# Kernel optimization log

Hardware: AMD Instinct MI355X
Metric: run time of the kernel (lower is better)

## Reference

```python
import jax, jax.numpy as jnp
import numpy as np
from jax import lax

B, T0, H0, W0 = 8, 8, 14, 14
C, NH = 768, 8
D = C // NH            # head_dim = 96
N = T0 * H0 * W0 + 1   # 1569 tokens incl. cls
SCALE = D ** -0.5
EPS = 1e-5


def _pool_norm(xh, conv_w, ln_g, ln_b, thw, stride):
    """AttentionPool with depthwise conv3d + LayerNorm. xh: [B, NH, N, D]."""
    cls_tok, xs = xh[:, :, :1, :], xh[:, :, 1:, :]
    b, n, _, d = xs.shape
    t, h, w = thw
    # (b n) c t h w
    xs = xs.reshape(b * n, t, h, w, d).transpose(0, 4, 1, 2, 3)
    y = lax.conv_general_dilated(
        xs, conv_w, window_strides=stride,
        padding=[(1, 1), (1, 1), (1, 1)],
        feature_group_count=d,
        dimension_numbers=("NCDHW", "OIDHW", "NCDHW"))
    ot, oh, ow = y.shape[2], y.shape[3], y.shape[4]
    y = y.transpose(0, 2, 3, 4, 1).reshape(b, n, ot * oh * ow, d)
    y = jnp.concatenate([cls_tok, y], axis=2)
    mu = y.mean(-1, keepdims=True)
    var = y.var(-1, keepdims=True)
    y = (y - mu) * lax.rsqrt(var + EPS) * ln_g + ln_b
    return y, (ot, oh, ow)


def setup_inputs() -> dict:
    key = jax.random.key(0)
    ks = jax.random.split(key, 12)
    s = lambda fan: (1.0 / np.sqrt(fan))
    return {
        "x": jax.random.normal(ks[0], (B, N, C), jnp.float32),
        "W_qkv": jax.random.normal(ks[1], (C, 3 * C), jnp.float32) * s(C),
        "b_qkv": jnp.zeros((3 * C,), jnp.float32),
        "W_proj": jax.random.normal(ks[2], (C, C), jnp.float32) * s(C),
        "b_proj": jnp.zeros((C,), jnp.float32),
        "conv_q_w": jax.random.normal(ks[3], (D, 1, 3, 3, 3), jnp.float32) * s(27),
        "conv_k_w": jax.random.normal(ks[4], (D, 1, 3, 3, 3), jnp.float32) * s(27),
        "conv_v_w": jax.random.normal(ks[5], (D, 1, 3, 3, 3), jnp.float32) * s(27),
        "lnq_g": jnp.ones((D,), jnp.float32), "lnq_b": jnp.zeros((D,), jnp.float32),
        "lnk_g": jnp.ones((D,), jnp.float32), "lnk_b": jnp.zeros((D,), jnp.float32),
        "lnv_g": jnp.ones((D,), jnp.float32), "lnv_b": jnp.zeros((D,), jnp.float32),
        "t": T0, "h": H0, "w": W0,
    }


def reference(x, W_qkv, b_qkv, W_proj, b_proj,
              conv_q_w, conv_k_w, conv_v_w,
              lnq_g, lnq_b, lnk_g, lnk_b, lnv_g, lnv_b,
              t, h, w):
    thw = (int(t), int(h), int(w))
    Bx, Nx, Cx = x.shape
    qkv = x @ W_qkv + b_qkv                       # [B, N, 3C]
    qkv = qkv.reshape(Bx, Nx, 3, NH, D).transpose(2, 0, 3, 1, 4)  # qkv b h n d
    q, k, v = qkv[0], qkv[1], qkv[2]
    q, q_shape = _pool_norm(q, conv_q_w, lnq_g, lnq_b, thw, (1, 1, 1))
    k, _ = _pool_norm(k, conv_k_w, lnk_g, lnk_b, thw, (1, 2, 2))
    v, _ = _pool_norm(v, conv_v_w, lnv_g, lnv_b, thw, (1, 2, 2))
    dots = jnp.einsum("bhid,bhjd->bhij", q, k) * SCALE
    attn = jax.nn.softmax(dots, axis=-1)
    out = jnp.einsum("bhij,bhjd->bhid", attn, v)  # [B, NH, Nq, D]
    out = out.transpose(0, 2, 1, 3).reshape(Bx, -1, Cx)
    out = out @ W_proj + b_proj
    return out
```

## Files before the change

### kernel.cpp

```cpp
#include <hip/hip_runtime.h>
#include <hip/hip_bf16.h>
#include <math.h>

#define B_   8
#define NH_  8
#define D_   96
#define C_   768
#define N_   1569
#define NKV_ 393
#define M_   (B_*N_)
#define QKV1 ((size_t)B_*NH_*N_*D_)
#define QPAD 1664
#define KPAD 416
#define SCALE_ 0.10206207261596575f

using short8v = __attribute__((ext_vector_type(8))) short;
using f32x4   = __attribute__((ext_vector_type(4))) float;
using f32x2   = __attribute__((ext_vector_type(2))) float;
typedef unsigned short u16;

#define GLOAD_LDS16(g, l) __builtin_amdgcn_global_load_lds( \
    (const __attribute__((address_space(1))) void*)(g),     \
    (__attribute__((address_space(3))) void*)(l), 16, 0, 0)

static __device__ __forceinline__ u16 f2bf(float f) {
    __hip_bfloat16 b = __float2bfloat16(f);
    return *(u16*)&b;
}

static __device__ __forceinline__ unsigned xcd_swizzle(unsigned orig, unsigned nwg) {
    const unsigned qq = nwg >> 3, rr = nwg & 7;
    const unsigned xcd = orig & 7, loc = orig >> 3;
    return (xcd < rr ? xcd * (qq + 1) : rr * (qq + 1) + (xcd - rr) * qq) + loc;
}

__global__ __launch_bounds__(256)
void cvt_f32_to_bf16(const float* __restrict__ in, u16* __restrict__ out, int n4)
{
    const int i = blockIdx.x * 256 + threadIdx.x;
    if (i < n4) {
        const float4 v = ((const float4*)in)[i];
        ushort4 o;
        o.x = f2bf(v.x); o.y = f2bf(v.y); o.z = f2bf(v.z); o.w = f2bf(v.w);
        ((ushort4*)out)[i] = o;
    }
}

__global__ __launch_bounds__(256)
void transpose_cvt(const float* __restrict__ W, u16* __restrict__ Wt, int ncols)
{
    __shared__ float tile[32][33];
    const int tx = threadIdx.x & 31, ty = threadIdx.x >> 5;
    const int n0 = blockIdx.x * 32, k0 = blockIdx.y * 32;
    #pragma unroll
    for (int i = 0; i < 4; ++i)
        tile[ty + i * 8][tx] = W[(size_t)(k0 + ty + i * 8) * ncols + n0 + tx];
    __syncthreads();
    #pragma unroll
    for (int i = 0; i < 4; ++i)
        Wt[(size_t)(n0 + ty + i * 8) * 768 + k0 + tx] = f2bf(tile[tx][ty + i * 8]);
}

__global__ __launch_bounds__(256)
void transpose_w(const float* __restrict__ cwq, const float* __restrict__ cwk,
                 const float* __restrict__ cwv, float* __restrict__ outT)
{
    const int i = blockIdx.x * 256 + threadIdx.x;
    if (i < 3 * 27 * 96) {
        const int tsr = i / 2592;
        const int r = i - tsr * 2592;
        const int tap = r / 96, ch = r - tap * 96;
        const float* src = tsr == 0 ? cwq : (tsr == 1 ? cwk : cwv);
        outT[i] = src[ch * 27 + tap];
    }
}

__global__ __launch_bounds__(256)
void zero_pad_vt(u16* __restrict__ vt)
{
    const int i = blockIdx.x * 256 + threadIdx.x;
    const int total = 64 * 96 * (KPAD - NKV_);
    if (i < total) {
        const int j = i % (KPAD - NKV_);
        const int rest = i / (KPAD - NKV_);
        vt[(size_t)rest * KPAD + NKV_ + j] = 0;
    }
}

template<int NC, bool SCATTER>
__global__ __launch_bounds__(512)
void gemm_bf16_kernel(const u16* __restrict__ A, const u16* __restrict__ Bt,
                      const float* __restrict__ bias, void* __restrict__ outp)
{
    constexpr int NXT = NC / 128;
    __shared__ alignas(16) u16 As[2][128 * 64];
    __shared__ alignas(16) u16 Bs[2][128 * 64];

    const int tid  = threadIdx.x;
    const int w    = tid >> 6, lane = tid & 63;
    const int c    = lane & 15, g = lane >> 4;
    const int wm   = w >> 2, wn = w & 3;
    const int lrow = lane >> 3, lcol = lane & 7;

    const unsigned wg = xcd_swizzle(blockIdx.x, gridDim.x);
    const int m0 = (int)(wg / NXT) * 128;
    const int n0 = (int)(wg % NXT) * 128;

    f32x4 acc[4][2];
    #pragma unroll
    for (int i = 0; i < 4; ++i)
        #pragma unroll
        for (int j = 0; j < 2; ++j) acc[i][j] = (f32x4){0.f, 0.f, 0.f, 0.f};

#define STAGE(BUF, K0) do {                                                      \
    _Pragma("unroll")                                                            \
    for (int t = 0; t < 2; ++t) {                                                \
        const int r = t * 64 + w * 8;                                            \
        const int row = r + lrow;                                                \
        const int scol = (lcol ^ (row & 7)) * 8;                                 \
        int m = m0 + row; if (m >= M_) m = M_ - 1;                               \
        GLOAD_LDS16(&A[(size_t)m * 768 + (K0) + scol], &As[BUF][r * 64]);        \
        GLOAD_LDS16(&Bt[(size_t)(n0 + row) * 768 + (K0) + scol],                 \
                    &Bs[BUF][r * 64]);                                           \
    } } while (0)

    const int xora = (g ^ (c & 7)) * 8;
    const int xorb = ((4 + g) ^ (c & 7)) * 8;

#define KSTEP(BUF, LAST, PREF, KNEXT) do {                                       \
    if (LAST) asm volatile("s_waitcnt vmcnt(0)" ::: "memory");                   \
    else      asm volatile("s_waitcnt vmcnt(4)" ::: "memory");                   \
    __builtin_amdgcn_s_barrier();                                                \
    short8v a0[4], a1[4], b0[2], b1[2];                                          \
    _Pragma("unroll")                                                            \
    for (int i = 0; i < 4; ++i) {                                                \
        const int ra = (wm * 64 + i * 16 + c) * 64;                              \
        a0[i] = *(const short8v*)&As[BUF][ra + xora];                            \
        a1[i] = *(const short8v*)&As[BUF][ra + xorb];                            \
    }                                                                            \
    _Pragma("unroll")                                                            \
    for (int j = 0; j < 2; ++j) {                                                \
        const int rb = (wn * 32 + j * 16 + c) * 64;                              \
        b0[j] = *(const short8v*)&Bs[BUF][rb + xora];                            \
        b1[j] = *(const short8v*)&Bs[BUF][rb + xorb];                            \
    }                                                                            \
    asm volatile("s_waitcnt lgkmcnt(0)" ::: "memory");                           \
    __builtin_amdgcn_sched_barrier(0);                                           \
    __builtin_amdgcn_s_barrier();                                                \
    if (PREF) STAGE(BUF, KNEXT);                                                 \
    __builtin_amdgcn_s_setprio(1);                                               \
    _Pragma("unroll")                                                            \
    for (int i = 0; i < 4; ++i)                                                  \
        _Pragma("unroll")                                                        \
        for (int j = 0; j < 2; ++j)                                              \
            acc[i][j] = __builtin_amdgcn_mfma_f32_16x16x32_bf16(                 \
                a0[i], b0[j], acc[i][j], 0, 0, 0);                               \
    _Pragma("unroll")                                                            \
    for (int i = 0; i < 4; ++i)                                                  \
        _Pragma("unroll")                                                        \
        for (int j = 0; j < 2; ++j)                                              \
            acc[i][j] = __builtin_amdgcn_mfma_f32_16x16x32_bf16(                 \
                a1[i], b1[j], acc[i][j], 0, 0, 0);                               \
    __builtin_amdgcn_s_setprio(0);                                               \
    } while (0)

    STAGE(0, 0);
    STAGE(1, 64);
    #pragma unroll
    for (int tt = 0; tt < 5; ++tt) {
        KSTEP(0, false, true, (2 * tt + 2) * 64);
        KSTEP(1, false, true, (2 * tt + 3) * 64);
    }
    KSTEP(0, false, false, 0);
    KSTEP(1, true,  false, 0);
#undef STAGE
#undef KSTEP

    #pragma unroll
    for (int i = 0; i < 4; ++i) {
        const int mrow = m0 + wm * 64 + i * 16 + g * 4;
        #pragma unroll
        for (int j = 0; j < 2; ++j) {
            const int ncol = n0 + wn * 32 + j * 16 + c;
            const float bv = bias[ncol];
            if constexpr (SCATTER) {
                u16* out = (u16*)outp;
                const int s   = ncol / C_;
                const int rem = ncol - s * C_;
                const int hh  = rem / D_;
                const int dd  = rem - hh * D_;
                #pragma unroll
                for (int r = 0; r < 4; ++r) {
                    const int m = mrow + r;
                    if (m < M_) {
                        const int bb2 = m / N_;
                        const int n = m - bb2 * N_;
                        out[(size_t)s * QKV1 +
                            ((size_t)(bb2 * NH_ + hh) * N_ + n) * D_ + dd] = f2bf(acc[i][j][r] + bv);
                    }
                }
            } else {
                float* out = (float*)outp;
                #pragma unroll
                for (int r = 0; r < 4; ++r) {
                    const int m = mrow + r;
                    if (m < M_) out[(size_t)m * NC + ncol] = acc[i][j][r] + bv;
                }
            }
        }
    }
}

static __device__ __forceinline__ void loadx6(const u16* __restrict__ rowp,
                                              int iw, f32x2 x[3])
{
    if (iw < 0 || iw >= 14) {
        x[0] = x[1] = x[2] = (f32x2){0.f, 0.f};
        return;
    }
    const unsigned* p = (const unsigned*)(rowp + (size_t)iw * 96);
    #pragma unroll
    for (int j = 0; j < 3; ++j) {
        const unsigned u = p[j];
        x[j][0] = __uint_as_float(u << 16);
        x[j][1] = __uint_as_float(u & 0xffff0000u);
    }
}

template<int STRIDE, int OHW, int WMODE, int WO0>
static __device__ __forceinline__
void pool_task(const u16* __restrict__ in, const float* __restrict__ cwT,
               const float* __restrict__ g, const float* __restrict__ bta,
               u16* __restrict__ out, int tokstride, int bh, int to, int ho,
               float oscale)
{
    const int sl = threadIdx.x & 15;
    const u16* base = in + (size_t)bh * N_ * 96 + 6 * sl;

    f32x2 acc[7][3];
    #pragma unroll
    for (int i = 0; i < 7; ++i)
        #pragma unroll
        for (int p = 0; p < 3; ++p) acc[i][p] = (f32x2){0.f, 0.f};

    #pragma unroll
    for (int dt = 0; dt < 3; ++dt) {
        const int t = to - 1 + dt;
        if (t < 0 || t > 7) continue;
        #pragma unroll
        for (int dh = 0; dh < 3; ++dh) {
            const int h = ho * STRIDE - 1 + dh;
            if (h < 0 || h >= 14) continue;
            const int tapb = dt * 9 + dh * 3;
            f32x2 wt[3][3];
            #pragma unroll
            for (int dw = 0; dw < 3; ++dw)
                #pragma unroll
                for (int p = 0; p < 3; ++p)
                    wt[dw][p] = *(const f32x2*)&cwT[(tapb + dw) * 96 + 6 * sl + 2 * p];
            const u16* rowp = base + (size_t)(1 + t * 196 + h * 14) * 96;

            if constexpr (STRIDE == 1) {
                f32x2 xm[3], x0[3], xp[3];
                loadx6(rowp, WO0 - 1, xm);
                loadx6(rowp, WO0, x0);
                #pragma unroll
                for (int wo = 0; wo < 7; ++wo) {
                    loadx6(rowp, WO0 + wo + 1, xp);
                    #pragma unroll
                    for (int p = 0; p < 3; ++p) {
                        acc[wo][p] = __builtin_elementwise_fma(wt[0][p], xm[p], acc[wo][p]);
                        acc[wo][p] = __builtin_elementwise_fma(wt[1][p], x0[p], acc[wo][p]);
                        acc[wo][p] = __builtin_elementwise_fma(wt[2][p], xp[p], acc[wo][p]);
                        xm[p] = x0[p]; x0[p] = xp[p];
                    }
                }
            } else {
                #pragma unroll
                for (int wo = 0; wo < 7; ++wo) {
                    #pragma unroll
                    for (int dw = 0; dw < 3; ++dw) {
                        f32x2 xa[3];
                        loadx6(rowp, 2 * wo - 1 + dw, xa);
                        #pragma unroll
                        for (int p = 0; p < 3; ++p)
                            acc[wo][p] = __builtin_elementwise_fma(wt[dw][p], xa[p], acc[wo][p]);
                    }
                }
            }
        }
    }

    f32x2 gg[3], bb[3];
    #pragma unroll
    for (int p = 0; p < 3; ++p) {
        gg[p] = *(const f32x2*)&g[6 * sl + 2 * p] * oscale;
        bb[p] = *(const f32x2*)&bta[6 * sl + 2 * p] * oscale;
    }

    #pragma unroll
    for (int wo = 0; wo < 7; ++wo) {
        float s = acc[wo][0][0] + acc[wo][0][1] + acc[wo][1][0] + acc[wo][1][1]
                + acc[wo][2][0] + acc[wo][2][1];
        float sq = acc[wo][0][0] * acc[wo][0][0];
        sq = fmaf(acc[wo][0][1], acc[wo][0][1], sq);
        sq = fmaf(acc[wo][1][0], acc[wo][1][0], sq);
        sq = fmaf(acc[wo][1][1], acc[wo][1][1], sq);
        sq = fmaf(acc[wo][2][0], acc[wo][2][0], sq);
        sq = fmaf(acc[wo][2][1], acc[wo][2][1], sq);
        #pragma unroll
        for (int off = 1; off < 16; off <<= 1) {
            s  += __shfl_xor(s, off, 64);
            sq += __shfl_xor(sq, off, 64);
        }
        const float mu = s * (1.f / 96.f);
        const float rstd = rsqrtf(sq * (1.f / 96.f) - mu * mu + 1e-5f);
        const f32x2 muv = (f32x2){mu, mu};
        const int tok = 1 + (to * OHW + ho) * OHW + WO0 + wo;
        u16 yb[6];
        #pragma unroll
        for (int p = 0; p < 3; ++p) {
            const f32x2 y = (acc[wo][p] - muv) * rstd * gg[p] + bb[p];
            yb[2 * p] = f2bf(y[0]); yb[2 * p + 1] = f2bf(y[1]);
        }
        if constexpr (WMODE == 2) {
            #pragma unroll
            for (int j = 0; j < 6; ++j)
                out[((size_t)bh * 96 + 6 * sl + j) * KPAD + tok] = yb[j];
        } else {
            unsigned* op = (unsigned*)&out[((size_t)bh * tokstride + tok) * 96 + 6 * sl];
            #pragma unroll
            for (int p = 0; p < 3; ++p)
                op[p] = (unsigned)yb[2 * p] | ((unsigned)yb[2 * p + 1] << 16);
        }
    }
}

template<int WMODE>
static __device__ __forceinline__
void pool_cls_v5(const u16* __restrict__ in, const float* __restrict__ g,
                 const float* __restrict__ bta, u16* __restrict__ out,
                 int tokstride, int bh, float oscale)
{
    const int sl = threadIdx.x & 15;
    const unsigned* p = (const unsigned*)(in + (size_t)bh * N_ * 96 + 6 * sl);
    f32x2 v[3];
    #pragma unroll
    for (int j = 0; j < 3; ++j) {
        const unsigned u = p[j];
        v[j][0] = __uint_as_float(u << 16);
        v[j][1] = __uint_as_float(u & 0xffff0000u);
    }
    float s = v[0][0] + v[0][1] + v[1][0] + v[1][1] + v[2][0] + v[2][1];
    float sq = v[0][0]*v[0][0] + v[0][1]*v[0][1] + v[1][0]*v[1][0]
             + v[1][1]*v[1][1] + v[2][0]*v[2][0] + v[2][1]*v[2][1];
    #pragma unroll
    for (int off = 1; off < 16; off <<= 1) {
        s  += __shfl_xor(s, off, 64);
        sq += __shfl_xor(sq, off, 64);
    }
    const float mu = s * (1.f / 96.f);
    const float rstd = rsqrtf(sq * (1.f / 96.f) - mu * mu + 1e-5f);
    u16 yb[6];
    #pragma unroll
    for (int p2 = 0; p2 < 3; ++p2) {
        const f32x2 gg = *(const f32x2*)&g[6 * sl + 2 * p2] * oscale;
        const f32x2 bb = *(const f32x2*)&bta[6 * sl + 2 * p2] * oscale;
        const f32x2 y = (v[p2] - (f32x2){mu, mu}) * rstd * gg + bb;
        yb[2 * p2] = f2bf(y[0]); yb[2 * p2 + 1] = f2bf(y[1]);
    }
    if constexpr (WMODE == 2) {
        #pragma unroll
        for (int j = 0; j < 6; ++j)
            out[((size_t)bh * 96 + 6 * sl + j) * KPAD] = yb[j];
    } else {
        unsigned* op = (unsigned*)&out[(size_t)bh * tokstride * 96 + 6 * sl];
        #pragma unroll
        for (int p2 = 0; p2 < 3; ++p2)
            op[p2] = (unsigned)yb[2 * p2] | ((unsigned)yb[2 * p2 + 1] << 16);
    }
}

#define NTASKS 21696
__global__ __launch_bounds__(256)
void pool_ln_v5_kernel(const u16* __restrict__ qin, const u16* __restrict__ kin,
                       const u16* __restrict__ vin, const float* __restrict__ cwT,
                       const float* __restrict__ gq, const float* __restrict__ bq,
                       const float* __restrict__ gk, const float* __restrict__ bk,
                       const float* __restrict__ gv, const float* __restrict__ bv,
                       u16* __restrict__ qout, u16* __restrict__ kout,
                       u16* __restrict__ vtout)
{
    const unsigned wg = xcd_swizzle(blockIdx.x, gridDim.x);
    const int gid = (int)(wg * 16 + (threadIdx.x >> 4));
    if (gid >= NTASKS) return;

    if (gid < 14336) {
        const int chunk = gid / 7168;
        const int r = gid - chunk * 7168;
        const int ho = r % 14;
        const int to = (r / 14) & 7;
        const int bh = r / 112;
        if (chunk == 0)
            pool_task<1, 14, 0, 0>(qin, cwT, gq, bq, qout, QPAD, bh, to, ho, SCALE_);
        else
            pool_task<1, 14, 0, 7>(qin, cwT, gq, bq, qout, QPAD, bh, to, ho, SCALE_);
    } else if (gid < 17920) {
        const int r = gid - 14336;
        const int ho = r % 7;
        const int to = (r / 7) & 7;
        const int bh = r / 56;
        pool_task<2, 7, 0, 0>(kin, cwT + 2592, gk, bk, kout, KPAD, bh, to, ho, 1.f);
    } else if (gid < 21504) {
        const int r = gid - 17920;
        const int ho = r % 7;
        const int to = (r / 7) & 7;
        const int bh = r / 56;
        pool_task<2, 7, 2, 0>(vin, cwT + 5184, gv, bv, vtout, KPAD, bh, to, ho, 1.f);
    } else {
        const int r = gid - 21504;
        const int tsr = r >> 6, bh = r & 63;
        if (tsr == 0)      pool_cls_v5<0>(qin, gq, bq, qout, QPAD, bh, SCALE_);
        else if (tsr == 1) pool_cls_v5<0>(kin, gk, bk, kout, KPAD, bh, 1.f);
        else               pool_cls_v5<2>(vin, gv, bv, vtout, KPAD, bh, 1.f);
    }
}

__global__ __launch_bounds__(256)
void attn_mfma_kernel(const u16* __restrict__ Q, const u16* __restrict__ K,
                      const u16* __restrict__ VT, u16* __restrict__ Out)
{
    __shared__ alignas(16) u16 plds[4][2][512];
    const int tid  = threadIdx.x;
    const int w    = tid >> 6, lane = tid & 63;
    const int c    = lane & 15, g = lane >> 4;

    const unsigned wg = xcd_swizzle(blockIdx.x, gridDim.x);
    const int bh = (int)(wg / 13);
    const int b  = bh >> 3, hh = bh & 7;
    const int q0 = (int)(wg % 13) * 128 + w * 32;

    const size_t qbase = (size_t)bh * QPAD * 96;
    const size_t kbase = (size_t)bh * KPAD * 96;

    short8v qa[2][3];
    #pragma unroll
    for (int s2 = 0; s2 < 2; ++s2)
        #pragma unroll
        for (int kf = 0; kf < 3; ++kf)
            qa[s2][kf] = *(const short8v*)
                &Q[qbase + (size_t)(q0 + s2 * 16 + c) * 96 + kf * 32 + g * 8];

    f32x4 oacc[2][6];
    #pragma unroll
    for (int s2 = 0; s2 < 2; ++s2)
        #pragma unroll
        for (int t = 0; t < 6; ++t) oacc[s2][t] = (f32x4){0.f, 0.f, 0.f, 0.f};
    float lsum[2][4] = {{0.f,0.f,0.f,0.f},{0.f,0.f,0.f,0.f}};

    short8v kb[2][6];
#define LOADK(IDX, PR) do {                                                     \
    _Pragma("unroll")                                                           \
    for (int h = 0; h < 2; ++h)                                                 \
        _Pragma("unroll")                                                       \
        for (int kf = 0; kf < 3; ++kf)                                          \
            kb[IDX][h * 3 + kf] = *(const short8v*)                             \
                &K[kbase + (size_t)((PR) * 32 + h * 16 + c) * 96 + kf * 32 + g * 8]; \
    } while (0)

    LOADK(0, 0);

    #pragma unroll
    for (int pr = 0; pr < 13; ++pr) {
        const int cur = pr & 1, nxt = cur ^ 1;

        short8v vt[6];
        #pragma unroll
        for (int t = 0; t < 6; ++t)
            vt[t] = *(const short8v*)
                &VT[kbase + (size_t)(t * 16 + c) * KPAD + pr * 32 + g * 8];

        f32x4 sacc[2][2];
        __builtin_amdgcn_s_setprio(1);
        #pragma unroll
        for (int s2 = 0; s2 < 2; ++s2)
            #pragma unroll
            for (int h = 0; h < 2; ++h) {
                f32x4 sa = (f32x4){0.f, 0.f, 0.f, 0.f};
                sa = __builtin_amdgcn_mfma_f32_16x16x32_bf16(qa[s2][0], kb[cur][h*3+0], sa, 0, 0, 0);
                sa = __builtin_amdgcn_mfma_f32_16x16x32_bf16(qa[s2][1], kb[cur][h*3+1], sa, 0, 0, 0);
                sa = __builtin_amdgcn_mfma_f32_16x16x32_bf16(qa[s2][2], kb[cur][h*3+2], sa, 0, 0, 0);
                sacc[s2][h] = sa;
            }
        __builtin_amdgcn_s_setprio(0);

        if (pr < 12) LOADK(nxt, pr + 1);

        #pragma unroll
        for (int s2 = 0; s2 < 2; ++s2)
            #pragma unroll
            for (int h = 0; h < 2; ++h) {
                const int jcol = pr * 32 + h * 16 + c;
                #pragma unroll
                for (int r = 0; r < 4; ++r) {
                    float s = sacc[s2][h][r];
                    if (jcol >= NKV_) s = -1e30f;
                    const float p = __expf(s);
                    lsum[s2][r] += p;
                    const int q    = g * 4 + r;
                    const int j    = h * 16 + c;
                    const int dstL = q | ((j >> 3) << 4);
                    plds[w][s2][dstL * 8 + (j & 7)] = f2bf(p);
                }
            }
        asm volatile("s_waitcnt lgkmcnt(0)" ::: "memory");
        __builtin_amdgcn_sched_barrier(0);
        const short8v pa0 = *(const short8v*)&plds[w][0][lane * 8];
        const short8v pa1 = *(const short8v*)&plds[w][1][lane * 8];

        __builtin_amdgcn_s_setprio(1);
        #pragma unroll
        for (int t = 0; t < 6; ++t)
            oacc[0][t] = __builtin_amdgcn_mfma_f32_16x16x32_bf16(pa0, vt[t], oacc[0][t], 0, 0, 0);
        #pragma unroll
        for (int t = 0; t < 6; ++t)
            oacc[1][t] = __builtin_amdgcn_mfma_f32_16x16x32_bf16(pa1, vt[t], oacc[1][t], 0, 0, 0);
        __builtin_amdgcn_s_setprio(0);
    }
#undef LOADK

    float linv[2][4];
    #pragma unroll
    for (int s2 = 0; s2 < 2; ++s2)
        #pragma unroll
        for (int r = 0; r < 4; ++r) {
            float s = lsum[s2][r];
            s += __shfl_xor(s, 1, 64);
            s += __shfl_xor(s, 2, 64);
            s += __shfl_xor(s, 4, 64);
            s += __shfl_xor(s, 8, 64);
            linv[s2][r] = 1.f / s;
        }

    #pragma unroll
    for (int s2 = 0; s2 < 2; ++s2)
        #pragma unroll
        for (int t = 0; t < 6; ++t)
            #pragma unroll
            for (int r = 0; r < 4; ++r) {
                const int row = q0 + s2 * 16 + g * 4 + r;
                if (row < N_)
                    Out[((size_t)(b * N_ + row)) * 768 + hh * 96 + t * 16 + c] =
                        f2bf(oacc[s2][t][r] * linv[s2][r]);
            }
}

extern "C" void kernel_launch(void* const* d_in, const int* in_sizes, int n_in,
                              void* d_out, int out_size, void* d_ws, size_t ws_size,
                              hipStream_t stream)
{
    const float* x     = (const float*)d_in[0];
    const float* Wqkv  = (const float*)d_in[1];
    const float* bqkv  = (const float*)d_in[2];
    const float* Wproj = (const float*)d_in[3];
    const float* bproj = (const float*)d_in[4];
    const float* cwq   = (const float*)d_in[5];
    const float* cwk   = (const float*)d_in[6];
    const float* cwv   = (const float*)d_in[7];
    const float* lnqg  = (const float*)d_in[8];
    const float* lnqb  = (const float*)d_in[9];
    const float* lnkg  = (const float*)d_in[10];
    const float* lnkb  = (const float*)d_in[11];
    const float* lnvg  = (const float*)d_in[12];
    const float* lnvb  = (const float*)d_in[13];

    u16* ws = (u16*)d_ws;
    u16* qkv_raw = ws;
    u16* q16 = qkv_raw + 3 * QKV1;
    u16* k16 = q16 + (size_t)64 * QPAD * 96;
    u16* vt16 = k16 + (size_t)64 * KPAD * 96;
    u16* x16    = vt16 + (size_t)64 * KPAD * 96;
    u16* Wqkvt  = x16 + (size_t)M_ * 768;
    u16* Wprojt = Wqkvt + (size_t)2304 * 768;
    float* cwT  = (float*)(Wprojt + (size_t)768 * 768);
    u16* attn16 = qkv_raw;
    float* out = (float*)d_out;

    cvt_f32_to_bf16<<<(M_ * 768 / 4 + 255) / 256, 256, 0, stream>>>(x, x16, M_ * 768 / 4);
    transpose_cvt<<<dim3(2304 / 32, 768 / 32), 256, 0, stream>>>(Wqkv, Wqkvt, 2304);
    transpose_cvt<<<dim3(768 / 32, 768 / 32), 256, 0, stream>>>(Wproj, Wprojt, 768);
    transpose_w<<<(3 * 27 * 96 + 255) / 256, 256, 0, stream>>>(cwq, cwk, cwv, cwT);
    zero_pad_vt<<<(64 * 96 * (KPAD - NKV_) + 255) / 256, 256, 0, stream>>>(vt16);

    gemm_bf16_kernel<2304, true><<<18 * 99, 512, 0, stream>>>(x16, Wqkvt, bqkv, qkv_raw);

    pool_ln_v5_kernel<<<(NTASKS + 15) / 16, 256, 0, stream>>>(
        qkv_raw, qkv_raw + QKV1, qkv_raw + 2 * QKV1, cwT,
        lnqg, lnqb, lnkg, lnkb, lnvg, lnvb, q16, k16, vt16);

    attn_mfma_kernel<<<13 * 64, 256, 0, stream>>>(q16, k16, vt16, attn16);

    gemm_bf16_kernel<768, false><<<6 * 99, 512, 0, stream>>>(attn16, Wprojt, bproj, out);
}
```

Measured before the change: 206.3 us.

## Merge prep kernels into one launch and interleave softmax with PV MFMAs

```diff
diff --git a/kernel.cpp b/kernel.cpp
--- a/kernel.cpp
+++ b/kernel.cpp
@@ -34,56 +34,72 @@
     return (xcd < rr ? xcd * (qq + 1) : rr * (qq + 1) + (xcd - rr) * qq) + loc;
 }
 
+#define PREP_CVT_B   9414
+#define PREP_WQ_B    1728
+#define PREP_WP_B    576
+#define PREP_WT_B    31
+#define PREP_ZP_B    552
+#define PREP_BLOCKS  (PREP_CVT_B + PREP_WQ_B + PREP_WP_B + PREP_WT_B + PREP_ZP_B)
+
+static __device__ __forceinline__
+void tile_transpose(const float* __restrict__ W, u16* __restrict__ Wt,
+                    int ncols, int n0, int k0, float* tile )
+{
+    const int tx = threadIdx.x & 31, ty = threadIdx.x >> 5;
+    #pragma unroll
+    for (int i = 0; i < 4; ++i)
+        tile[(ty + i * 8) * 33 + tx] = W[(size_t)(k0 + ty + i * 8) * ncols + n0 + tx];
+    __syncthreads();
+    #pragma unroll
+    for (int i = 0; i < 4; ++i)
+        Wt[(size_t)(n0 + ty + i * 8) * 768 + k0 + tx] = f2bf(tile[tx * 33 + ty + i * 8]);
+}
+
 __global__ __launch_bounds__(256)
-void cvt_f32_to_bf16(const float* __restrict__ in, u16* __restrict__ out, int n4)
-{
-    const int i = blockIdx.x * 256 + threadIdx.x;
-    if (i < n4) {
-        const float4 v = ((const float4*)in)[i];
-        ushort4 o;
-        o.x = f2bf(v.x); o.y = f2bf(v.y); o.z = f2bf(v.z); o.w = f2bf(v.w);
-        ((ushort4*)out)[i] = o;
-    }
-}
-
-__global__ __launch_bounds__(256)
-void transpose_cvt(const float* __restrict__ W, u16* __restrict__ Wt, int ncols)
-{
-    __shared__ float tile[32][33];
-    const int tx = threadIdx.x & 31, ty = threadIdx.x >> 5;
-    const int n0 = blockIdx.x * 32, k0 = blockIdx.y * 32;
-    #pragma unroll
-    for (int i = 0; i < 4; ++i)
-        tile[ty + i * 8][tx] = W[(size_t)(k0 + ty + i * 8) * ncols + n0 + tx];
-    __syncthreads();
-    #pragma unroll
-    for (int i = 0; i < 4; ++i)
-        Wt[(size_t)(n0 + ty + i * 8) * 768 + k0 + tx] = f2bf(tile[tx][ty + i * 8]);
-}
-
-__global__ __launch_bounds__(256)
-void transpose_w(const float* __restrict__ cwq, const float* __restrict__ cwk,
-                 const float* __restrict__ cwv, float* __restrict__ outT)
-{
-    const int i = blockIdx.x * 256 + threadIdx.x;
-    if (i < 3 * 27 * 96) {
-        const int tsr = i / 2592;
-        const int r = i - tsr * 2592;
-        const int tap = r / 96, ch = r - tap * 96;
-        const float* src = tsr == 0 ? cwq : (tsr == 1 ? cwk : cwv);
-        outT[i] = src[ch * 27 + tap];
-    }
-}
-
-__global__ __launch_bounds__(256)
-void zero_pad_vt(u16* __restrict__ vt)
-{
-    const int i = blockIdx.x * 256 + threadIdx.x;
-    const int total = 64 * 96 * (KPAD - NKV_);
-    if (i < total) {
-        const int j = i % (KPAD - NKV_);
-        const int rest = i / (KPAD - NKV_);
-        vt[(size_t)rest * KPAD + NKV_ + j] = 0;
+void prep_kernel(const float* __restrict__ x, const float* __restrict__ Wqkv,
+                 const float* __restrict__ Wproj,
+                 const float* __restrict__ cwq, const float* __restrict__ cwk,
+                 const float* __restrict__ cwv,
+                 u16* __restrict__ x16, u16* __restrict__ Wqkvt,
+                 u16* __restrict__ Wprojt, float* __restrict__ cwT,
+                 u16* __restrict__ vt16)
+{
+    __shared__ float tile[32 * 33];
+    const int bid = blockIdx.x;
+    const int tid = threadIdx.x;
+
+    if (bid < PREP_CVT_B) {
+        const int i = bid * 256 + tid;
+        const int n4 = M_ * 768 / 4;
+        if (i < n4) {
+            const float4 v = ((const float4*)x)[i];
+            ushort4 o;
+            o.x = f2bf(v.x); o.y = f2bf(v.y); o.z = f2bf(v.z); o.w = f2bf(v.w);
+            ((ushort4*)x16)[i] = o;
+        }
+    } else if (bid < PREP_CVT_B + PREP_WQ_B) {
+        const int b2 = bid - PREP_CVT_B;
+        tile_transpose(Wqkv, Wqkvt, 2304, (b2 % 72) * 32, (b2 / 72) * 32, tile);
+    } else if (bid < PREP_CVT_B + PREP_WQ_B + PREP_WP_B) {
+        const int b2 = bid - PREP_CVT_B - PREP_WQ_B;
+        tile_transpose(Wproj, Wprojt, 768, (b2 % 24) * 32, (b2 / 24) * 32, tile);
+    } else if (bid < PREP_CVT_B + PREP_WQ_B + PREP_WP_B + PREP_WT_B) {
+        const int i = (bid - PREP_CVT_B - PREP_WQ_B - PREP_WP_B) * 256 + tid;
+        if (i < 3 * 27 * 96) {
+            const int tsr = i / 2592;
+            const int r = i - tsr * 2592;
+            const int tap = r / 96, ch = r - tap * 96;
+            const float* src = tsr == 0 ? cwq : (tsr == 1 ? cwk : cwv);
+            cwT[i] = src[ch * 27 + tap];
+        }
+    } else {
+        const int i = (bid - PREP_CVT_B - PREP_WQ_B - PREP_WP_B - PREP_WT_B) * 256 + tid;
+        const int total = 64 * 96 * (KPAD - NKV_);
+        if (i < total) {
+            const int j = i % (KPAD - NKV_);
+            const int rest = i / (KPAD - NKV_);
+            vt16[(size_t)rest * KPAD + NKV_ + j] = 0;
+        }
     }
 }
 
@@ -497,35 +513,56 @@
         if (pr < 12) LOADK(nxt, pr + 1);
 
         #pragma unroll
-        for (int s2 = 0; s2 < 2; ++s2)
-            #pragma unroll
-            for (int h = 0; h < 2; ++h) {
-                const int jcol = pr * 32 + h * 16 + c;
-                #pragma unroll
-                for (int r = 0; r < 4; ++r) {
-                    float s = sacc[s2][h][r];
-                    if (jcol >= NKV_) s = -1e30f;
-                    const float p = __expf(s);
-                    lsum[s2][r] += p;
-                    const int q    = g * 4 + r;
-                    const int j    = h * 16 + c;
-                    const int dstL = q | ((j >> 3) << 4);
-                    plds[w][s2][dstL * 8 + (j & 7)] = f2bf(p);
-                }
+        for (int h = 0; h < 2; ++h) {
+            const int jcol = pr * 32 + h * 16 + c;
+            #pragma unroll
+            for (int r = 0; r < 4; ++r) {
+                float s = sacc[0][h][r];
+                if (jcol >= NKV_) s = -1e30f;
+                const float p = __expf(s);
+                lsum[0][r] += p;
+                const int q    = g * 4 + r;
+                const int j    = h * 16 + c;
+                const int dstL = q | ((j >> 3) << 4);
+                plds[w][0][dstL * 8 + (j & 7)] = f2bf(p);
             }
+        }
         asm volatile("s_waitcnt lgkmcnt(0)" ::: "memory");
         __builtin_amdgcn_sched_barrier(0);
-        const short8v pa0 = *(const short8v*)&plds[w][0][lane * 8];
-        const short8v pa1 = *(const short8v*)&plds[w][1][lane * 8];
-
-        __builtin_amdgcn_s_setprio(1);
-        #pragma unroll
-        for (int t = 0; t < 6; ++t)
-            oacc[0][t] = __builtin_amdgcn_mfma_f32_16x16x32_bf16(pa0, vt[t], oacc[0][t], 0, 0, 0);
-        #pragma unroll
-        for (int t = 0; t < 6; ++t)
-            oacc[1][t] = __builtin_amdgcn_mfma_f32_16x16x32_bf16(pa1, vt[t], oacc[1][t], 0, 0, 0);
-        __builtin_amdgcn_s_setprio(0);
+        {
+            const short8v pa0 = *(const short8v*)&plds[w][0][lane * 8];
+            __builtin_amdgcn_s_setprio(1);
+            #pragma unroll
+            for (int t = 0; t < 6; ++t)
+                oacc[0][t] = __builtin_amdgcn_mfma_f32_16x16x32_bf16(pa0, vt[t], oacc[0][t], 0, 0, 0);
+            __builtin_amdgcn_s_setprio(0);
+        }
+
+        #pragma unroll
+        for (int h = 0; h < 2; ++h) {
+            const int jcol = pr * 32 + h * 16 + c;
+            #pragma unroll
+            for (int r = 0; r < 4; ++r) {
+                float s = sacc[1][h][r];
+                if (jcol >= NKV_) s = -1e30f;
+                const float p = __expf(s);
+                lsum[1][r] += p;
+                const int q    = g * 4 + r;
+                const int j    = h * 16 + c;
+                const int dstL = q | ((j >> 3) << 4);
+                plds[w][1][dstL * 8 + (j & 7)] = f2bf(p);
+            }
+        }
+        asm volatile("s_waitcnt lgkmcnt(0)" ::: "memory");
+        __builtin_amdgcn_sched_barrier(0);
+        {
+            const short8v pa1 = *(const short8v*)&plds[w][1][lane * 8];
+            __builtin_amdgcn_s_setprio(1);
+            #pragma unroll
+            for (int t = 0; t < 6; ++t)
+                oacc[1][t] = __builtin_amdgcn_mfma_f32_16x16x32_bf16(pa1, vt[t], oacc[1][t], 0, 0, 0);
+            __builtin_amdgcn_s_setprio(0);
+        }
     }
 #undef LOADK
 
@@ -586,11 +623,8 @@
     u16* attn16 = qkv_raw;
     float* out = (float*)d_out;
 
-    cvt_f32_to_bf16<<<(M_ * 768 / 4 + 255) / 256, 256, 0, stream>>>(x, x16, M_ * 768 / 4);
-    transpose_cvt<<<dim3(2304 / 32, 768 / 32), 256, 0, stream>>>(Wqkv, Wqkvt, 2304);
-    transpose_cvt<<<dim3(768 / 32, 768 / 32), 256, 0, stream>>>(Wproj, Wprojt, 768);
-    transpose_w<<<(3 * 27 * 96 + 255) / 256, 256, 0, stream>>>(cwq, cwk, cwv, cwT);
-    zero_pad_vt<<<(64 * 96 * (KPAD - NKV_) + 255) / 256, 256, 0, stream>>>(vt16);
+    prep_kernel<<<PREP_BLOCKS, 256, 0, stream>>>(
+        x, Wqkv, Wproj, cwq, cwk, cwv, x16, Wqkvt, Wprojt, cwT, vt16);
 
     gemm_bf16_kernel<2304, true><<<18 * 99, 512, 0, stream>>>(x16, Wqkvt, bqkv, qkv_raw);
 
```

New measurement: 199.2 us. -3.4%, faster.
